# Performance work log

Measured on AMD Instinct MI355X. Metric: run time of the kernel, lower is better.

Reference implementation:

```python
import jax, jax.numpy as jnp
import numpy as np

P = 2        # patch size (all 3 dims)
NB = 8       # num_bands
N = 16       # d_state
DTR = 8      # dt_rank = d_model // 16
DCONV = 4    # d_conv
SMAX = 2.0   # smax_dt = smax_B = smax_C


def _ln(x, g, b):
    mu = x.mean(-1, keepdims=True)
    v = ((x - mu) ** 2).mean(-1, keepdims=True)
    return (x - mu) / jnp.sqrt(v + 1e-5) * g + b


def _silu(x):
    return x * jax.nn.sigmoid(x)


def _ssm_layer(x, band, m, rho, Win, bin_, convw, convb, Wx, Wdt, bdt, Alog, Dp,
               Wout, bout, edt, eB, eC, wr, wm):
    # x: [B, L, d_model] -> bidirectional conditioned selective scan (BiFCSSM)
    Bsz, L, _ = x.shape
    ED = convw.shape[0]
    xz = x @ Win + bin_
    xp, z = xz[..., :ED], xz[..., ED:]
    # depthwise causal conv1d over L
    xpad = jnp.pad(xp, ((0, 0), (DCONV - 1, 0), (0, 0)))
    xc = sum(xpad[:, k:k + L, :] * convw[:, k] for k in range(DCONV)) + convb
    xc = _silu(xc)
    dbl = xc @ Wx                                    # [B,L,DTR+2N]
    dt = jax.nn.softplus(dbl[..., :DTR] @ Wdt + bdt)  # [B,L,ED]
    # band/radius/mask conditioned modulation of delta, B, C
    s_dt = SMAX * jax.nn.sigmoid(edt[band][None] + wr[0] * rho[None] + wm[0] * m)
    s_B = SMAX * jax.nn.sigmoid(eB[band][None] + wr[1] * rho[None] + wm[1] * m)
    s_C = SMAX * jax.nn.sigmoid(eC[band][None] + wr[2] * rho[None] + wm[2] * m)
    dt = dt * s_dt[..., None]
    Bm = dbl[..., DTR:DTR + N] * s_B[..., None]       # [B,L,N]
    Cm = dbl[..., DTR + N:] * s_C[..., None]          # [B,L,N]
    A = -jnp.exp(Alog)                                # [ED,N]
    dA = jnp.exp(dt[..., None] * A)                   # [B,L,ED,N]
    dBu = (dA - 1.0) / A * Bm[:, :, None, :] * xc[..., None]   # exact ZOH
    dA_s = jnp.moveaxis(dA, 1, 0)
    dBu_s = jnp.moveaxis(dBu, 1, 0)
    C_s = jnp.moveaxis(Cm, 1, 0)
    h0 = jnp.zeros((Bsz, ED, N), x.dtype)

    def step(h, inp):
        a, bu, c = inp
        h = a * h + bu
        return h, jnp.einsum('ben,bn->be', h, c)

    _, yf = jax.lax.scan(step, h0, (dA_s, dBu_s, C_s))
    _, yb = jax.lax.scan(step, h0, (dA_s, dBu_s, C_s), reverse=True)
    y = jnp.moveaxis(yf + yb, 0, 1) + Dp * xc
    y = y * _silu(z)
    return y @ Wout + bout


def _fwd(kspace_ri, mask, pe_w, pe_b, pu_w, pu_b, ln_g, ln_b, fn_g, fn_b,
         cond_band, cond_rad_w, cond_mask_w, l0_Win, l0_bin, l0_convw, l0_convb,
         l0_Wx, l0_Wdt, l0_bdt, l0_Alog, l0_D, l0_Wout, l0_bout, l0_edt, l0_eB,
         l0_eC, l0_wr, l0_wm):
    Bsz, C, nx, ny, nz = kspace_ri.shape
    gx, gy, gz = nx // P, ny // P, nz // P
    L = gx * gy * gz
    # patch embed (Conv3d, kernel==stride) as blocked einsum
    xr = kspace_ri.reshape(Bsz, C, gx, P, gy, P, gz, P)
    x = jnp.einsum('bcxiyjzk,dcijk->bdxyz', xr, pe_w) + pe_b[None, :, None, None, None]
    DM = x.shape[1]
    x = x.reshape(Bsz, DM, L).transpose(0, 2, 1)               # [B,L,D]
    m = mask.reshape(Bsz, 1, gx, P, gy, P, gz, P).mean(axis=(3, 5, 7)).reshape(Bsz, L)
    m = jnp.clip(m, 0.0, 1.0)
    # raster scan ordering: identity permutation, rho_bar, band ids
    rho = jnp.arange(L, dtype=x.dtype) / float(L - 1)
    band = jnp.clip(jnp.floor(rho * NB).astype(jnp.int32), 0, NB - 1)
    # condition tokens
    cond = cond_band[band][None] + rho[None, :, None] * cond_rad_w + m[:, :, None] * cond_mask_w
    h = _ln(x + cond, ln_g, ln_b)
    h = h + _ssm_layer(_ln(h, fn_g, fn_b), band, m, rho, l0_Win, l0_bin, l0_convw,
                       l0_convb, l0_Wx, l0_Wdt, l0_bdt, l0_Alog, l0_D, l0_Wout,
                       l0_bout, l0_edt, l0_eB, l0_eC, l0_wr, l0_wm)
    # patch unembed (ConvTranspose3d, kernel==stride) as blocked einsum
    hg = h.transpose(0, 2, 1).reshape(Bsz, DM, gx, gy, gz)
    out = jnp.einsum('bdxyz,dcijk->bcxiyjzk', hg, pu_w).reshape(Bsz, C, nx, ny, nz)
    out = out + pu_b[None, :, None, None, None]
    return kspace_ri + out


def setup_inputs() -> dict:
    key = jax.random.key(0)
    ks = jax.random.split(key, 24)
    ED, DM, CIN = 256, 128, 16

    def nrm(k, shape, s):
        return jax.random.normal(k, shape, jnp.float32) * s

    return {
        'kspace_ri': jax.random.normal(ks[0], (1, CIN, 64, 64, 16), jnp.float32),
        'mask': jax.random.uniform(ks[1], (1, 1, 64, 64, 16), jnp.float32),
        'pe_w': nrm(ks[2], (DM, CIN, P, P, P), 0.09),
        'pe_b': nrm(ks[3], (DM,), 0.02),
        'pu_w': nrm(ks[4], (DM, CIN, P, P, P), 0.05),
        'pu_b': jnp.zeros((CIN,), jnp.float32),
        'ln_g': jnp.ones((DM,), jnp.float32),
        'ln_b': jnp.zeros((DM,), jnp.float32),
        'fn_g': jnp.ones((DM,), jnp.float32),
        'fn_b': jnp.zeros((DM,), jnp.float32),
        'cond_band': nrm(ks[5], (NB, DM), 0.02),
        'cond_rad_w': nrm(ks[6], (DM,), 0.02),
        'cond_mask_w': nrm(ks[7], (DM,), 0.02),
        'l0_Win': nrm(ks[8], (DM, 2 * ED), 0.05),
        'l0_bin': jnp.zeros((2 * ED,), jnp.float32),
        'l0_convw': nrm(ks[9], (ED, DCONV), 0.2),
        'l0_convb': jnp.zeros((ED,), jnp.float32),
        'l0_Wx': nrm(ks[10], (ED, DTR + 2 * N), 0.05),
        'l0_Wdt': nrm(ks[11], (DTR, ED), 0.1),
        'l0_bdt': jnp.full((ED,), -3.0, jnp.float32),
        'l0_Alog': jnp.log(jnp.tile(jnp.arange(1, N + 1, dtype=jnp.float32), (ED, 1))),
        'l0_D': jnp.ones((ED,), jnp.float32),
        'l0_Wout': nrm(ks[12], (ED, DM), 0.05),
        'l0_bout': jnp.zeros((DM,), jnp.float32),
        'l0_edt': nrm(ks[13], (NB,), 0.1),
        'l0_eB': nrm(ks[14], (NB,), 0.1),
        'l0_eC': nrm(ks[15], (NB,), 0.1),
        'l0_wr': nrm(ks[16], (3,), 0.1),
        'l0_wm': nrm(ks[17], (3,), 0.1),
    }


def reference(kspace_ri, mask, pe_w, pe_b, pu_w, pu_b, ln_g, ln_b, fn_g, fn_b,
              cond_band, cond_rad_w, cond_mask_w, l0_Win, l0_bin, l0_convw,
              l0_convb, l0_Wx, l0_Wdt, l0_bdt, l0_Alog, l0_D, l0_Wout, l0_bout,
              l0_edt, l0_eB, l0_eC, l0_wr, l0_wm):
    return _fwd(kspace_ri, mask, pe_w, pe_b, pu_w, pu_b, ln_g, ln_b, fn_g, fn_b,
                cond_band, cond_rad_w, cond_mask_w, l0_Win, l0_bin, l0_convw,
                l0_convb, l0_Wx, l0_Wdt, l0_bdt, l0_Alog, l0_D, l0_Wout, l0_bout,
                l0_edt, l0_eB, l0_eC, l0_wr, l0_wm)
```

## Files before the change

### kernel.cpp

```cpp
#include <hip/hip_runtime.h>
#include <hip/hip_bf16.h>

#define L_TOK 8192
#define NCh 256
#define CLh 32
#define LOG2E 1.44269504088896f

typedef short bf16x8 __attribute__((ext_vector_type(8)));
typedef float f32x4 __attribute__((ext_vector_type(4)));

static __device__ __forceinline__ float nexp2(float x) {
#if __has_builtin(__builtin_amdgcn_exp2f)
    return __builtin_amdgcn_exp2f(x);
#else
    return exp2f(x);
#endif
}
static __device__ __forceinline__ float sigm(float x) {
    return 1.f / (1.f + nexp2(-x * LOG2E));
}

static __device__ __forceinline__ ushort f2bf(float x) {
    union { float f; uint u; } v; v.f = x;
    uint r = v.u + 0x7fffu + ((v.u >> 16) & 1u);
    return (ushort)(r >> 16);
}
static __device__ __forceinline__ float bf2f(ushort h) {
    union { float f; uint u; } v; v.u = ((uint)h) << 16;
    return v.f;
}
static __device__ __forceinline__ void f2hl(float x, ushort* hi, ushort* lo) {
    ushort h = f2bf(x);
    *hi = h;
    *lo = f2bf(x - bf2f(h));
}

// ... 41 lines not shown
        if (n < 256) {
            float s = 0.f;
#pragma unroll
            for (int r = 0; r < 8; ++r) s += Wx[k * 40 + r] * Wdt[r * 256 + n];
            v = s;
        } else if (n < 288) {
            v = Wx[k * 40 + 8 + (n - 256)];
        } else {
            v = 0.f;
        }
    }
    ushort h, lo; f2hl(v, &h, &lo);
    wH[i] = h; wL[i] = lo;
}

__global__ __launch_bounds__(256) void embed_ln_k(const float* __restrict__ ks,
                                                  const ushort* __restrict__ wH, const ushort* __restrict__ wL,
                                                  const float* __restrict__ pe_b, const float* __restrict__ cond_band,
                                                  const float* __restrict__ cond_rad, const float* __restrict__ cond_mask,
                                                  const float* __restrict__ mbuf,
                                                  const float* __restrict__ ln_g, const float* __restrict__ ln_b,
                                                  const float* __restrict__ fn_g, const float* __restrict__ fn_b,
                                                  float* __restrict__ h_,
                                                  ushort* __restrict__ hnH, ushort* __restrict__ hnL) {
    __shared__ __align__(16) char smem[41472];
    ushort (*AsH)[72] = (ushort(*)[72])(smem);
    ushort (*AsL)[72] = (ushort(*)[72])(smem + 2304);
    ushort (*BsH)[72] = (ushort(*)[72])(smem + 4608);
    ushort (*BsL)[72] = (ushort(*)[72])(smem + 23040);
    float  (*Cs)[132] = (float(*)[132])(smem);

    const int tid = threadIdx.x;
    const int lane = tid & 63, wn = tid >> 6;
    const int ln = lane & 15, q = lane >> 4;
    const int mb = blockIdx.x * 16;

    f32x4 acc[2];
    acc[0] = (f32x4){0.f, 0.f, 0.f, 0.f};
    acc[1] = (f32x4){0.f, 0.f, 0.f, 0.f};

    for (int kc = 0; kc < 128; kc += 64) {
        __syncthreads();
        for (int u = tid; u < 1024; u += 256) {
            int r = u >> 6, kk = u & 63;
            int l = mb + r, k = kc + kk;
            int cc = k >> 3, ijk = k & 7;
            int xg = l >> 8, yg = (l >> 3) & 31, zg = l & 7;
            int i2 = (ijk >> 2) & 1, j2 = (ijk >> 1) & 1, k2 = ijk & 1;
// ... 2 lines not shown
            AsH[r][kk] = h; AsL[r][kk] = lo;
        }
        for (int u = tid; u < 1024; u += 256) {
            int n = u >> 3, g = u & 7;
            *(uint4*)&BsH[n][g * 8] = *(const uint4*)&wH[W_PE + n * 128 + kc + g * 8];
            *(uint4*)&BsL[n][g * 8] = *(const uint4*)&wL[W_PE + n * 128 + kc + g * 8];
        }
        __syncthreads();
#pragma unroll
        for (int ks_ = 0; ks_ < 64; ks_ += 32) {
            const int kk = ks_ + q * 8;
            bf16x8 ah = *(const bf16x8*)&AsH[ln][kk];
            bf16x8 al = *(const bf16x8*)&AsL[ln][kk];
#pragma unroll
            for (int cb = 0; cb < 2; ++cb) {
                bf16x8 bh = *(const bf16x8*)&BsH[wn * 32 + cb * 16 + ln][kk];
                bf16x8 bl = *(const bf16x8*)&BsL[wn * 32 + cb * 16 + ln][kk];
                acc[cb] = __builtin_amdgcn_mfma_f32_16x16x32_bf16(ah, bh, acc[cb], 0, 0, 0);
                acc[cb] = __builtin_amdgcn_mfma_f32_16x16x32_bf16(ah, bl, acc[cb], 0, 0, 0);
                acc[cb] = __builtin_amdgcn_mfma_f32_16x16x32_bf16(al, bh, acc[cb], 0, 0, 0);
            }
        }
    }
    __syncthreads();
#pragma unroll
    for (int cb = 0; cb < 2; ++cb) {
#pragma unroll
        for (int r = 0; r < 4; ++r) {
            int row = q * 4 + r;
            int col = wn * 32 + cb * 16 + ln;
            int l = mb + row;
            float rho = (float)l * (1.0f / 8191.0f);
            int band = min(7, (int)(rho * 8.0f));
            Cs[row][col] = acc[cb][r] + pe_b[col] + cond_band[band * 128 + col]
                           + rho * cond_rad[col] + mbuf[l] * cond_mask[col];
        }
    }
    __syncthreads();
    {
        int row = tid >> 4, j = tid & 15;
        int l = mb + row;
        float v8[8];
        float s = 0.f, s2 = 0.f;
#pragma unroll
        for (int i = 0; i < 8; ++i) {
// ... 9 lines not shown
        s = 0.f; s2 = 0.f;
#pragma unroll
        for (int i = 0; i < 8; ++i) {
            int col = j * 8 + i;
            float h = (v8[i] - mu) * rstd * ln_g[col] + ln_b[col];
            hv[i] = h; s += h; s2 += h * h;
        }
#pragma unroll
        for (int i = 0; i < 8; i += 4)
            *(float4*)&h_[(size_t)l * 128 + j * 8 + i] = make_float4(hv[i], hv[i + 1], hv[i + 2], hv[i + 3]);
#pragma unroll
        for (int o = 1; o < 16; o <<= 1) { s += __shfl_xor(s, o, 16); s2 += __shfl_xor(s2, o, 16); }
        mu = s * (1.f / 128.f);
        var = s2 * (1.f / 128.f) - mu * mu;
        rstd = rsqrtf(fmaxf(var, 0.f) + 1e-5f);
        union { ushort u[8]; uint4 v4; } oh, ol;
#pragma unroll
        for (int i = 0; i < 8; ++i) {
            int col = j * 8 + i;
            float o2 = (hv[i] - mu) * rstd * fn_g[col] + fn_b[col];
            ushort hh, ll; f2hl(o2, &hh, &ll);
            oh.u[i] = hh; ol.u[i] = ll;
        }
        *(uint4*)&hnH[(size_t)l * 128 + j * 8] = oh.v4;
        *(uint4*)&hnL[(size_t)l * 128 + j * 8] = ol.v4;
    }
}

__global__ __launch_bounds__(256) void win_k(const ushort* __restrict__ Ah, const ushort* __restrict__ Al,
                                             const ushort* __restrict__ wH, const ushort* __restrict__ wL,
                                             const float* __restrict__ bin_,
                                             float* __restrict__ xp, float* __restrict__ sz) {
    __shared__ ushort AsH[64][72], AsL[64][72];
    __shared__ ushort BsH[64][72], BsL[64][72];
    const int tid = threadIdx.x;
    const int lane = tid & 63, wave = tid >> 6;
    const int wm = wave & 1, wn = wave >> 1;
    const int ln = lane & 15, q = lane >> 4;
    const int mb = blockIdx.x * 64, nb = blockIdx.y * 64;

    f32x4 acc[2][2];
#pragma unroll
    for (int rb = 0; rb < 2; ++rb)
#pragma unroll
        for (int cb = 0; cb < 2; ++cb) acc[rb][cb] = (f32x4){0.f, 0.f, 0.f, 0.f};

    for (int kc = 0; kc < 128; kc += 64) {
        __syncthreads();
        for (int u = tid; u < 512; u += 256) {
            int r = u >> 3, g = u & 7;
            size_t go = (size_t)(mb + r) * 128 + kc + g * 8;
            *(uint4*)&AsH[r][g * 8] = *(const uint4*)&Ah[go];
            *(uint4*)&AsL[r][g * 8] = *(const uint4*)&Al[go];
        }
        for (int u = tid; u < 512; u += 256) {
            int n = u >> 3, g = u & 7;
            size_t go = (size_t)(W_WIN) + (size_t)(nb + n) * 128 + kc + g * 8;
            *(uint4*)&BsH[n][g * 8] = *(const uint4*)&wH[go];
            *(uint4*)&BsL[n][g * 8] = *(const uint4*)&wL[go];
        }
        __syncthreads();
#pragma unroll
        for (int ks_ = 0; ks_ < 64; ks_ += 32) {
            const int kk = ks_ + q * 8;
            bf16x8 ah[2], al[2], bh[2], bl[2];
#pragma unroll
            for (int rb = 0; rb < 2; ++rb) {
                ah[rb] = *(const bf16x8*)&AsH[wm * 32 + rb * 16 + ln][kk];
                al[rb] = *(const bf16x8*)&AsL[wm * 32 + rb * 16 + ln][kk];
            }
#pragma unroll
            for (int cb = 0; cb < 2; ++cb) {
                bh[cb] = *(const bf16x8*)&BsH[wn * 32 + cb * 16 + ln][kk];
                bl[cb] = *(const bf16x8*)&BsL[wn * 32 + cb * 16 + ln][kk];
            }
#pragma unroll
            for (int rb = 0; rb < 2; ++rb)
#pragma unroll
                for (int cb = 0; cb < 2; ++cb) {
                    acc[rb][cb] = __builtin_amdgcn_mfma_f32_16x16x32_bf16(ah[rb], bh[cb], acc[rb][cb], 0, 0, 0);
                    acc[rb][cb] = __builtin_amdgcn_mfma_f32_16x16x32_bf16(ah[rb], bl[cb], acc[rb][cb], 0, 0, 0);
                    acc[rb][cb] = __builtin_amdgcn_mfma_f32_16x16x32_bf16(al[rb], bh[cb], acc[rb][cb], 0, 0, 0);
                }
        }
    }
#pragma unroll
    for (int rb = 0; rb < 2; ++rb)
#pragma unroll
        for (int cb = 0; cb < 2; ++cb)
#pragma unroll
            for (int r = 0; r < 4; ++r) {
                int l = mb + wm * 32 + rb * 16 + q * 4 + r;
                int col = nb + wn * 32 + cb * 16 + ln;
                float v = acc[rb][cb][r] + bin_[col];
                if (col < 256) {
                    xp[(size_t)l * 256 + col] = v;
                } else {
                    sz[(size_t)l * 256 + (col - 256)] = v * sigm(v);
                }
            }
}

__global__ __launch_bounds__(256) void conv_k(const float* __restrict__ xp, const float* __restrict__ convw,
                                              const float* __restrict__ convb, float* __restrict__ xc) {
    int id = blockIdx.x * 256 + threadIdx.x;
    int l = id >> 6, e4 = (id & 63) * 4;
    float4 cw[4];
#pragma unroll
    for (int j = 0; j < 4; ++j) cw[j] = *(const float4*)&convw[(e4 + j) * 4];
    float4 cb = *(const float4*)&convb[e4];
    float o[4] = {cb.x, cb.y, cb.z, cb.w};
#pragma unroll
    for (int k = 0; k < 4; ++k) {
        int lp = l - 3 + k;
        if (lp >= 0) {
// ... 90 lines not shown
                if (col < 256) {
                    float sc0 = 2.0f * sigm(edt[band] + wr[0] * rho + wm[0] * mv);
                    float v2 = v + bdt[col];
                    float sp = (v2 > 20.f) ? v2 : log1pf(expf(v2));
                    dt[(size_t)l * 256 + col] = sp * sc0;
                } else if (col < 272) {
                    float sc1 = 2.0f * sigm(eB[band] + wr[1] * rho + wm[1] * mv);
                    Bm[(size_t)l * 16 + (col - 256)] = v * sc1;
                } else if (col < 288) {
                    float sc2 = 2.0f * sigm(eC[band] + wr[2] * rho + wm[2] * mv);
                    Cm[(size_t)l * 16 + (col - 272)] = v * sc2;
                }
            }
}

template <int PHASE>
__global__ __launch_bounds__(256) void scan_k(const float* __restrict__ dt, const float* __restrict__ xc,
                                              const float* __restrict__ Bm, const float* __restrict__ Cm,
                                              const float* __restrict__ Alog,
                                              float* __restrict__ Hb, float* __restrict__ sdtb,
                                              float* __restrict__ yf, float* __restrict__ yb) {
    const int c = blockIdx.x, dir = blockIdx.y, e = threadIdx.x;
    __shared__ float bms[CLh][16];
    __shared__ float cms[CLh][16];
    for (int idx = e; idx < CLh * 16; idx += 256) {
        bms[idx >> 4][idx & 15] = Bm[c * (CLh * 16) + idx];
        if (PHASE == 1) cms[idx >> 4][idx & 15] = Cm[c * (CLh * 16) + idx];
    }
    float A2[16], iv[16], h[16];
#pragma unroll
    for (int n = 0; n < 16; ++n) {
        float ea = nexp2(Alog[e * 16 + n] * LOG2E);
        A2[n] = -ea * LOG2E;
        iv[n] = -1.0f / ea;
    }
    const size_t hofs = (size_t)(dir * NCh + c) * 4096 + e * 16;
    if (PHASE == 0) {
#pragma unroll
        for (int n = 0; n < 16; ++n) h[n] = 0.f;
    } else {
#pragma unroll
        for (int j = 0; j < 4; ++j) {
            float4 hv = *(const float4*)&Hb[hofs + 4 * j];
            h[4 * j] = hv.x; h[4 * j + 1] = hv.y; h[4 * j + 2] = hv.z; h[4 * j + 3] = hv.w;
        }
    }
    const int base = c * CLh;
    float cu[8], cx[8], nu[8], nx[8];
#pragma unroll
    for (int j = 0; j < 8; ++j) {
        int p = dir ? (CLh - 1 - j) : j;
        cu[j] = dt[(size_t)(base + p) * 256 + e];
        cx[j] = xc[(size_t)(base + p) * 256 + e];
    }
    __syncthreads();
    float sdt = 0.f;
    float* __restrict__ yp = dir ? yb : yf;
#pragma unroll
    for (int g = 0; g < CLh / 8; ++g) {
        if (g + 1 < CLh / 8) {
#pragma unroll
            for (int j = 0; j < 8; ++j) {
                int s = (g + 1) * 8 + j;
                int p = dir ? (CLh - 1 - s) : s;
                nu[j] = dt[(size_t)(base + p) * 256 + e];
                nx[j] = xc[(size_t)(base + p) * 256 + e];
            }
        }
#pragma unroll
        for (int j = 0; j < 8; ++j) {
            int s = g * 8 + j;
            int p = dir ? (CLh - 1 - s) : s;
            float u = cu[j], xv = cx[j];
            union { float4 v[4]; float f[16]; } bb, cc;
            const float4* bp = (const float4*)&bms[p][0];
            bb.v[0] = bp[0]; bb.v[1] = bp[1]; bb.v[2] = bp[2]; bb.v[3] = bp[3];
            if (PHASE == 1) {
                const float4* cp = (const float4*)&cms[p][0];
                cc.v[0] = cp[0]; cc.v[1] = cp[1]; cc.v[2] = cp[2]; cc.v[3] = cp[3];
            }
            float y = 0.f;
#pragma unroll
            for (int n = 0; n < 16; ++n) {
                float a = nexp2(A2[n] * u);
                float w = xv * bb.f[n] * iv[n];
                float t = h[n] + w;
                h[n] = a * t - w;
                if (PHASE == 1) y += h[n] * cc.f[n];
            }
            if (PHASE == 0) sdt += u;
            if (PHASE == 1) yp[(size_t)(base + p) * 256 + e] = y;
        }
#pragma unroll
        for (int j = 0; j < 8; ++j) { cu[j] = nu[j]; cx[j] = nx[j]; }
    }
    if (PHASE == 0) {
#pragma unroll
        for (int j = 0; j < 4; ++j) {
            float4 hv = make_float4(h[4 * j], h[4 * j + 1], h[4 * j + 2], h[4 * j + 3]);
            *(float4*)&Hb[hofs + 4 * j] = hv;
        }
        if (dir == 0) sdtb[c * 256 + e] = sdt;
    }
}

__global__ __launch_bounds__(64) void combine_k(const float* __restrict__ Hb, float* __restrict__ Hpre,
                                                const float* __restrict__ sdtb, const float* __restrict__ Alog) {
    int id = blockIdx.x * 64 + threadIdx.x;
    int dir = id >> 12, en = id & 4095, e = en >> 4;
    float A2 = -nexp2(Alog[en] * LOG2E) * LOG2E;
    float hi = 0.f;
    for (int g = 0; g < NCh / 8; ++g) {
        float Pv[8], qv[8];
#pragma unroll
        for (int j = 0; j < 8; ++j) {
            int c = dir ? (NCh - 1 - (g * 8 + j)) : (g * 8 + j);
            Pv[j] = sdtb[c * 256 + e];
            qv[j] = Hb[(size_t)(dir * NCh + c) * 4096 + en];
        }
#pragma unroll
        for (int j = 0; j < 8; ++j) {
            int c = dir ? (NCh - 1 - (g * 8 + j)) : (g * 8 + j);
            float P = nexp2(A2 * Pv[j]);
            Hpre[(size_t)(dir * NCh + c) * 4096 + en] = hi;
            hi = P * hi + qv[j];
        }
    }
}

__global__ __launch_bounds__(256) void wout_k(const float* __restrict__ yf, const float* __restrict__ yb,
                                              const float* __restrict__ xc, const float* __restrict__ sz,
                                              const float* __restrict__ Dp,
                                              const ushort* __restrict__ wH, const ushort* __restrict__ wL,
                                              const float* __restrict__ bout, const float* __restrict__ h_,
                                              ushort* __restrict__ hfH, ushort* __restrict__ hfL) {
    __shared__ ushort AsH[32][72], AsL[32][72];
    __shared__ ushort BsH[64][72], BsL[64][72];
    const int tid = threadIdx.x;
    const int lane = tid & 63, wave = tid >> 6;
    const int wm = wave & 1, wn = wave >> 1;
    const int ln = lane & 15, q = lane >> 4;
    const int mb = blockIdx.x * 32, nb = blockIdx.y * 64;

    f32x4 acc[2];
    acc[0] = (f32x4){0.f, 0.f, 0.f, 0.f};
    acc[1] = (f32x4){0.f, 0.f, 0.f, 0.f};

    for (int kc = 0; kc < 256; kc += 64) {
        __syncthreads();
        for (int u = tid; u < 512; u += 256) {
            int r = u >> 4, kq = u & 15;
            size_t go = (size_t)(mb + r) * 256 + kc + kq * 4;
            float4 a = *(const float4*)&yf[go];
            float4 b = *(const float4*)&yb[go];
            float4 x = *(const float4*)&xc[go];
            float4 s = *(const float4*)&sz[go];
            float4 d = *(const float4*)&Dp[kc + kq * 4];
            float v0 = (a.x + b.x + d.x * x.x) * s.x;
            float v1 = (a.y + b.y + d.y * x.y) * s.y;
            float v2 = (a.z + b.z + d.z * x.z) * s.z;
            float v3 = (a.w + b.w + d.w * x.w) * s.w;
            union { ushort u[4]; uint2 v2; } hh, ll;
            f2hl(v0, &hh.u[0], &ll.u[0]); f2hl(v1, &hh.u[1], &ll.u[1]);
            f2hl(v2, &hh.u[2], &ll.u[2]); f2hl(v3, &hh.u[3], &ll.u[3]);
            *(uint2*)&AsH[r][kq * 4] = hh.v2;
            *(uint2*)&AsL[r][kq * 4] = ll.v2;
        }
        for (int u = tid; u < 512; u += 256) {
            int n = u >> 3, g = u & 7;
            size_t go = (size_t)(W_WOUT) + (size_t)(nb + n) * 256 + kc + g * 8;
            *(uint4*)&BsH[n][g * 8] = *(const uint4*)&wH[go];
            *(uint4*)&BsL[n][g * 8] = *(const uint4*)&wL[go];
        }
        __syncthreads();
#pragma unroll
        for (int ks_ = 0; ks_ < 64; ks_ += 32) {
            const int kk = ks_ + q * 8;
            bf16x8 ah = *(const bf16x8*)&AsH[wm * 16 + ln][kk];
            bf16x8 al = *(const bf16x8*)&AsL[wm * 16 + ln][kk];
#pragma unroll
            for (int cb = 0; cb < 2; ++cb) {
                bf16x8 bh = *(const bf16x8*)&BsH[wn * 32 + cb * 16 + ln][kk];
                bf16x8 bl = *(const bf16x8*)&BsL[wn * 32 + cb * 16 + ln][kk];
                acc[cb] = __builtin_amdgcn_mfma_f32_16x16x32_bf16(ah, bh, acc[cb], 0, 0, 0);
                acc[cb] = __builtin_amdgcn_mfma_f32_16x16x32_bf16(ah, bl, acc[cb], 0, 0, 0);
                acc[cb] = __builtin_amdgcn_mfma_f32_16x16x32_bf16(al, bh, acc[cb], 0, 0, 0);
            }
        }
    }
#pragma unroll
    for (int cb = 0; cb < 2; ++cb)
#pragma unroll
        for (int r = 0; r < 4; ++r) {
            int l = mb + wm * 16 + q * 4 + r;
            int col = nb + wn * 32 + cb * 16 + ln;
            float v = acc[cb][r] + bout[col] + h_[(size_t)l * 128 + col];
            ushort hh, ll; f2hl(v, &hh, &ll);
            hfH[(size_t)l * 128 + col] = hh;
            hfL[(size_t)l * 128 + col] = ll;
        }
}

__global__ __launch_bounds__(256) void unembed_k(const ushort* __restrict__ Ah, const ushort* __restrict__ Al,
                                                 const ushort* __restrict__ wH, const ushort* __restrict__ wL,
                                                 const float* __restrict__ pu_b, const float* __restrict__ ks,
                                                 float* __restrict__ out) {
    __shared__ ushort AsH[32][72], AsL[32][72];
    __shared__ ushort BsH[64][72], BsL[64][72];
    const int tid = threadIdx.x;
    const int lane = tid & 63, wave = tid >> 6;
    const int wm = wave & 1, wn = wave >> 1;
    const int ln = lane & 15, q = lane >> 4;
    const int mb = blockIdx.x * 32, nb = blockIdx.y * 64;

    f32x4 acc[2];
    acc[0] = (f32x4){0.f, 0.f, 0.f, 0.f};
    acc[1] = (f32x4){0.f, 0.f, 0.f, 0.f};

    for (int kc = 0; kc < 128; kc += 64) {
        __syncthreads();
        for (int u = tid; u < 256; u += 256) {
            int r = u >> 3, g = u & 7;
            size_t go = (size_t)(mb + r) * 128 + kc + g * 8;
            *(uint4*)&AsH[r][g * 8] = *(const uint4*)&Ah[go];
            *(uint4*)&AsL[r][g * 8] = *(const uint4*)&Al[go];
        }
        for (int u = tid; u < 512; u += 256) {
            int n = u >> 3, g = u & 7;
            size_t go = (size_t)(W_PU) + (size_t)(nb + n) * 128 + kc + g * 8;
            *(uint4*)&BsH[n][g * 8] = *(const uint4*)&wH[go];
            *(uint4*)&BsL[n][g * 8] = *(const uint4*)&wL[go];
        }
        __syncthreads();
#pragma unroll
        for (int ks_ = 0; ks_ < 64; ks_ += 32) {
            const int kk = ks_ + q * 8;
            bf16x8 ah = *(const bf16x8*)&AsH[wm * 16 + ln][kk];
            bf16x8 al = *(const bf16x8*)&AsL[wm * 16 + ln][kk];
#pragma unroll
            for (int cb = 0; cb < 2; ++cb) {
                bf16x8 bh = *(const bf16x8*)&BsH[wn * 32 + cb * 16 + ln][kk];
                bf16x8 bl = *(const bf16x8*)&BsL[wn * 32 + cb * 16 + ln][kk];
                acc[cb] = __builtin_amdgcn_mfma_f32_16x16x32_bf16(ah, bh, acc[cb], 0, 0, 0);
                acc[cb] = __builtin_amdgcn_mfma_f32_16x16x32_bf16(ah, bl, acc[cb], 0, 0, 0);
                acc[cb] = __builtin_amdgcn_mfma_f32_16x16x32_bf16(al, bh, acc[cb], 0, 0, 0);
            }
        }
    }
#pragma unroll
    for (int cb = 0; cb < 2; ++cb)
#pragma unroll
        for (int r = 0; r < 4; ++r) {
            int l = mb + wm * 16 + q * 4 + r;
            int col = nb + wn * 32 + cb * 16 + ln;
            int xg = l >> 8, yg = (l >> 3) & 31, zg = l & 7;
            int c = col >> 3, ijk = col & 7;
            int i2 = (ijk >> 2) & 1, j2 = (ijk >> 1) & 1, k2 = ijk & 1;
            size_t idx = (size_t)((c * 64 + 2 * xg + i2) * 64 + (2 * yg + j2)) * 16 + 2 * zg + k2;
            out[idx] = acc[cb][r] + pu_b[c] + ks[idx];
        }
}

extern "C" void kernel_launch(void* const* d_in, const int* in_sizes, int n_in,
                              void* d_out, int out_size, void* d_ws, size_t ws_size,
                              hipStream_t stream) {
    const float* ks    = (const float*)d_in[0];
    const float* mask  = (const float*)d_in[1];
    const float* pe_w  = (const float*)d_in[2];
    const float* pe_b  = (const float*)d_in[3];
    const float* pu_w  = (const float*)d_in[4];
    const float* pu_b  = (const float*)d_in[5];
    const float* ln_g  = (const float*)d_in[6];
    const float* ln_b  = (const float*)d_in[7];
    const float* fn_g  = (const float*)d_in[8];
    const float* fn_b  = (const float*)d_in[9];
// ... 13 lines not shown
    const float* bout  = (const float*)d_in[23];
    const float* edt   = (const float*)d_in[24];
    const float* eB    = (const float*)d_in[25];
    const float* eC    = (const float*)d_in[26];
    const float* wr    = (const float*)d_in[27];
    const float* wm    = (const float*)d_in[28];
    float* out = (float*)d_out;

    char* base = (char*)d_ws;
    size_t o = 0;
    auto alloc = [&](size_t bytes) { char* p = base + o; o += (bytes + 255) & ~(size_t)255; return p; };
    float*  mbuf = (float*)alloc(32768);
    ushort* wH   = (ushort*)alloc(W_TOT * 2);
    ushort* wL   = (ushort*)alloc(W_TOT * 2);
    float*  h_   = (float*)alloc(4194304);
    ushort* hnH  = (ushort*)alloc(2097152);
    ushort* hnL  = (ushort*)alloc(2097152);
    float*  xp   = (float*)alloc(8388608);
    float*  sz   = (float*)alloc(8388608);
    float*  xc   = (float*)alloc(8388608);
    float*  dt   = (float*)alloc(8388608);
    float*  Bm   = (float*)alloc(524288);
    float*  Cm   = (float*)alloc(524288);
    float*  Hb   = (float*)alloc(8388608);
    float*  Hpre = (float*)alloc(8388608);
    float*  sdtb = (float*)alloc(262144);
    float*  yf   = (float*)alloc(8388608);
    float*  yb   = (float*)alloc(8388608);
    ushort* hfH  = (ushort*)alloc(2097152);
    ushort* hfL  = (ushort*)alloc(2097152);

    prep_k<<<864, 256, 0, stream>>>(pe_w, Win, Wx, Wdt, Wout, pu_w, mask, wH, wL, mbuf);
    embed_ln_k<<<512, 256, 0, stream>>>(ks, wH, wL, pe_b, cond_band, cond_rad, cond_mask, mbuf,
                                        ln_g, ln_b, fn_g, fn_b, h_, hnH, hnL);
    win_k<<<dim3(128, 8), 256, 0, stream>>>(hnH, hnL, wH, wL, bin_, xp, sz);
    conv_k<<<2048, 256, 0, stream>>>(xp, convw, convb, xc);
    proj_k<<<dim3(128, 5), 256, 0, stream>>>(xc, wH, wL, bdt, mbuf, edt, eB, eC, wr, wm, dt, Bm, Cm);
    scan_k<0><<<dim3(NCh, 2), 256, 0, stream>>>(dt, xc, Bm, Cm, Alog, Hb, sdtb, nullptr, nullptr);
    combine_k<<<128, 64, 0, stream>>>(Hb, Hpre, sdtb, Alog);
    scan_k<1><<<dim3(NCh, 2), 256, 0, stream>>>(dt, xc, Bm, Cm, Alog, Hpre, sdtb, yf, yb);
    wout_k<<<dim3(256, 2), 256, 0, stream>>>(yf, yb, xc, sz, Dp, wH, wL, bout, h_, hfH, hfL);
    unembed_k<<<dim3(256, 2), 256, 0, stream>>>(hfH, hfL, wH, wL, pu_b, ks, out);
}
```

Baseline: 239.9 us.

## Fuse embed+Win GEMM and scan phase 1 with Wout and unembed GEMMs

Merges the embedding/LayerNorm kernel with the Win projection so normalized activations stay in shared memory instead of round-tripping through global hi/lo buffers. It also fuses the second scan phase with the output projection and unembedding in one 512-thread block per chunk, where both scan directions run concurrently and are summed in LDS. This removes the yf/yb/hn/hf intermediate buffers and three launches. In exchange, tail_k runs only 256 blocks with heavy register use, and it reads Wout/pu weights straight from global memory rather than staging them in shared memory.

```diff
diff --git a/kernel.cpp b/kernel.cpp
--- a/kernel.cpp
+++ b/kernel.cpp
@@ -19,7 +19,6 @@
 static __device__ __forceinline__ float sigm(float x) {
     return 1.f / (1.f + nexp2(-x * LOG2E));
 }
-
 static __device__ __forceinline__ ushort f2bf(float x) {
     union { float f; uint u; } v; v.f = x;
     uint r = v.u + 0x7fffu + ((v.u >> 16) & 1u);
@@ -91,24 +90,29 @@
     wH[i] = h; wL[i] = lo;
 }
 
-__global__ __launch_bounds__(256) void embed_ln_k(const float* __restrict__ ks,
-                                                  const ushort* __restrict__ wH, const ushort* __restrict__ wL,
-                                                  const float* __restrict__ pe_b, const float* __restrict__ cond_band,
-                                                  const float* __restrict__ cond_rad, const float* __restrict__ cond_mask,
-                                                  const float* __restrict__ mbuf,
-                                                  const float* __restrict__ ln_g, const float* __restrict__ ln_b,
-                                                  const float* __restrict__ fn_g, const float* __restrict__ fn_b,
-                                                  float* __restrict__ h_,
-                                                  ushort* __restrict__ hnH, ushort* __restrict__ hnL) {
-    __shared__ __align__(16) char smem[41472];
+__global__ __launch_bounds__(256) void front_k(const float* __restrict__ ks,
+                                               const ushort* __restrict__ wH, const ushort* __restrict__ wL,
+                                               const float* __restrict__ pe_b, const float* __restrict__ cond_band,
+                                               const float* __restrict__ cond_rad, const float* __restrict__ cond_mask,
+                                               const float* __restrict__ mbuf,
+                                               const float* __restrict__ ln_g, const float* __restrict__ ln_b,
+                                               const float* __restrict__ fn_g, const float* __restrict__ fn_b,
+                                               const float* __restrict__ bin_,
+                                               float* __restrict__ h_,
+                                               float* __restrict__ xp, float* __restrict__ sz) {
+    __shared__ __align__(16) char smem[51968];
     ushort (*AsH)[72] = (ushort(*)[72])(smem);
     ushort (*AsL)[72] = (ushort(*)[72])(smem + 2304);
     ushort (*BsH)[72] = (ushort(*)[72])(smem + 4608);
     ushort (*BsL)[72] = (ushort(*)[72])(smem + 23040);
-    float  (*Cs)[132] = (float(*)[132])(smem);
+    float  (*Cs)[132]  = (float(*)[132])(smem);
+    ushort (*hnH)[136] = (ushort(*)[136])(smem + 8448);
+    ushort (*hnL)[136] = (ushort(*)[136])(smem + 12800);
+    ushort (*BwH)[136] = (ushort(*)[136])(smem + 17152);
+    ushort (*BwL)[136] = (ushort(*)[136])(smem + 34560);
 
     const int tid = threadIdx.x;
-    const int lane = tid & 63, wn = tid >> 6;
+    const int lane = tid & 63, wv = tid >> 6;
     const int ln = lane & 15, q = lane >> 4;
     const int mb = blockIdx.x * 16;
 
@@ -141,8 +145,8 @@
             bf16x8 al = *(const bf16x8*)&AsL[ln][kk];
 #pragma unroll
             for (int cb = 0; cb < 2; ++cb) {
-                bf16x8 bh = *(const bf16x8*)&BsH[wn * 32 + cb * 16 + ln][kk];
-                bf16x8 bl = *(const bf16x8*)&BsL[wn * 32 + cb * 16 + ln][kk];
+                bf16x8 bh = *(const bf16x8*)&BsH[wv * 32 + cb * 16 + ln][kk];
+                bf16x8 bl = *(const bf16x8*)&BsL[wv * 32 + cb * 16 + ln][kk];
                 acc[cb] = __builtin_amdgcn_mfma_f32_16x16x32_bf16(ah, bh, acc[cb], 0, 0, 0);
                 acc[cb] = __builtin_amdgcn_mfma_f32_16x16x32_bf16(ah, bl, acc[cb], 0, 0, 0);
                 acc[cb] = __builtin_amdgcn_mfma_f32_16x16x32_bf16(al, bh, acc[cb], 0, 0, 0);
@@ -155,7 +159,7 @@
 #pragma unroll
         for (int r = 0; r < 4; ++r) {
             int row = q * 4 + r;
-            int col = wn * 32 + cb * 16 + ln;
+            int col = wv * 32 + cb * 16 + ln;
             int l = mb + row;
             float rho = (float)l * (1.0f / 8191.0f);
             int band = min(7, (int)(rho * 8.0f));
@@ -195,91 +199,47 @@
         mu = s * (1.f / 128.f);
         var = s2 * (1.f / 128.f) - mu * mu;
         rstd = rsqrtf(fmaxf(var, 0.f) + 1e-5f);
-        union { ushort u[8]; uint4 v4; } oh, ol;
 #pragma unroll
         for (int i = 0; i < 8; ++i) {
             int col = j * 8 + i;
             float o2 = (hv[i] - mu) * rstd * fn_g[col] + fn_b[col];
             ushort hh, ll; f2hl(o2, &hh, &ll);
-            oh.u[i] = hh; ol.u[i] = ll;
-        }
-        *(uint4*)&hnH[(size_t)l * 128 + j * 8] = oh.v4;
-        *(uint4*)&hnL[(size_t)l * 128 + j * 8] = ol.v4;
-    }
-}
-
-__global__ __launch_bounds__(256) void win_k(const ushort* __restrict__ Ah, const ushort* __restrict__ Al,
-                                             const ushort* __restrict__ wH, const ushort* __restrict__ wL,
-                                             const float* __restrict__ bin_,
-                                             float* __restrict__ xp, float* __restrict__ sz) {
-    __shared__ ushort AsH[64][72], AsL[64][72];
-    __shared__ ushort BsH[64][72], BsL[64][72];
-    const int tid = threadIdx.x;
-    const int lane = tid & 63, wave = tid >> 6;
-    const int wm = wave & 1, wn = wave >> 1;
-    const int ln = lane & 15, q = lane >> 4;
-    const int mb = blockIdx.x * 64, nb = blockIdx.y * 64;
-
-    f32x4 acc[2][2];
-#pragma unroll
-    for (int rb = 0; rb < 2; ++rb)
-#pragma unroll
-        for (int cb = 0; cb < 2; ++cb) acc[rb][cb] = (f32x4){0.f, 0.f, 0.f, 0.f};
-
-    for (int kc = 0; kc < 128; kc += 64) {
-        __syncthreads();
-        for (int u = tid; u < 512; u += 256) {
-            int r = u >> 3, g = u & 7;
-            size_t go = (size_t)(mb + r) * 128 + kc + g * 8;
-            *(uint4*)&AsH[r][g * 8] = *(const uint4*)&Ah[go];
-            *(uint4*)&AsL[r][g * 8] = *(const uint4*)&Al[go];
-        }
-        for (int u = tid; u < 512; u += 256) {
-            int n = u >> 3, g = u & 7;
-            size_t go = (size_t)(W_WIN) + (size_t)(nb + n) * 128 + kc + g * 8;
-            *(uint4*)&BsH[n][g * 8] = *(const uint4*)&wH[go];
-            *(uint4*)&BsL[n][g * 8] = *(const uint4*)&wL[go];
-        }
-        __syncthreads();
-#pragma unroll
-        for (int ks_ = 0; ks_ < 64; ks_ += 32) {
-            const int kk = ks_ + q * 8;
-            bf16x8 ah[2], al[2], bh[2], bl[2];
-#pragma unroll
-            for (int rb = 0; rb < 2; ++rb) {
-                ah[rb] = *(const bf16x8*)&AsH[wm * 32 + rb * 16 + ln][kk];
-                al[rb] = *(const bf16x8*)&AsL[wm * 32 + rb * 16 + ln][kk];
-            }
-#pragma unroll
-            for (int cb = 0; cb < 2; ++cb) {
-                bh[cb] = *(const bf16x8*)&BsH[wn * 32 + cb * 16 + ln][kk];
-                bl[cb] = *(const bf16x8*)&BsL[wn * 32 + cb * 16 + ln][kk];
-            }
-#pragma unroll
-            for (int rb = 0; rb < 2; ++rb)
-#pragma unroll
-                for (int cb = 0; cb < 2; ++cb) {
-                    acc[rb][cb] = __builtin_amdgcn_mfma_f32_16x16x32_bf16(ah[rb], bh[cb], acc[rb][cb], 0, 0, 0);
-                    acc[rb][cb] = __builtin_amdgcn_mfma_f32_16x16x32_bf16(ah[rb], bl[cb], acc[rb][cb], 0, 0, 0);
-                    acc[rb][cb] = __builtin_amdgcn_mfma_f32_16x16x32_bf16(al[rb], bh[cb], acc[rb][cb], 0, 0, 0);
-                }
-        }
-    }
-#pragma unroll
-    for (int rb = 0; rb < 2; ++rb)
-#pragma unroll
-        for (int cb = 0; cb < 2; ++cb)
-#pragma unroll
-            for (int r = 0; r < 4; ++r) {
-                int l = mb + wm * 32 + rb * 16 + q * 4 + r;
-                int col = nb + wn * 32 + cb * 16 + ln;
-                float v = acc[rb][cb][r] + bin_[col];
-                if (col < 256) {
-                    xp[(size_t)l * 256 + col] = v;
-                } else {
-                    sz[(size_t)l * 256 + (col - 256)] = v * sigm(v);
-                }
-            }
+            hnH[row][col] = hh; hnL[row][col] = ll;
+        }
+    }
+    for (int nt = 0; nt < 8; ++nt) {
+        __syncthreads();
+        for (int u = tid; u < 1024; u += 256) {
+            int n = u >> 4, g = u & 15;
+            size_t go = (size_t)(W_WIN) + (size_t)(nt * 64 + n) * 128 + g * 8;
+            *(uint4*)&BwH[n][g * 8] = *(const uint4*)&wH[go];
+            *(uint4*)&BwL[n][g * 8] = *(const uint4*)&wL[go];
+        }
+        __syncthreads();
+        f32x4 wa = (f32x4){0.f, 0.f, 0.f, 0.f};
+#pragma unroll
+        for (int kst = 0; kst < 4; ++kst) {
+            const int kk = kst * 32 + q * 8;
+            bf16x8 ah = *(const bf16x8*)&hnH[ln][kk];
+            bf16x8 al = *(const bf16x8*)&hnL[ln][kk];
+            bf16x8 bh = *(const bf16x8*)&BwH[wv * 16 + ln][kk];
+            bf16x8 bl = *(const bf16x8*)&BwL[wv * 16 + ln][kk];
+            wa = __builtin_amdgcn_mfma_f32_16x16x32_bf16(ah, bh, wa, 0, 0, 0);
+            wa = __builtin_amdgcn_mfma_f32_16x16x32_bf16(ah, bl, wa, 0, 0, 0);
+            wa = __builtin_amdgcn_mfma_f32_16x16x32_bf16(al, bh, wa, 0, 0, 0);
+        }
+#pragma unroll
+        for (int r = 0; r < 4; ++r) {
+            int l = mb + q * 4 + r;
+            int col = nt * 64 + wv * 16 + ln;
+            float v = wa[r] + bin_[col];
+            if (col < 256) {
+                xp[(size_t)l * 256 + col] = v;
+            } else {
+                sz[(size_t)l * 256 + (col - 256)] = v * sigm(v);
+            }
+        }
+    }
 }
 
 __global__ __launch_bounds__(256) void conv_k(const float* __restrict__ xp, const float* __restrict__ convw,
@@ -400,36 +360,20 @@
             }
 }
 
-template <int PHASE>
-__global__ __launch_bounds__(256) void scan_k(const float* __restrict__ dt, const float* __restrict__ xc,
-                                              const float* __restrict__ Bm, const float* __restrict__ Cm,
-                                              const float* __restrict__ Alog,
-                                              float* __restrict__ Hb, float* __restrict__ sdtb,
-                                              float* __restrict__ yf, float* __restrict__ yb) {
+__global__ __launch_bounds__(256) void scan0_k(const float* __restrict__ dt, const float* __restrict__ xc,
+                                               const float* __restrict__ Bm, const float* __restrict__ Alog,
+                                               float* __restrict__ Hb, float* __restrict__ sdtb) {
     const int c = blockIdx.x, dir = blockIdx.y, e = threadIdx.x;
     __shared__ float bms[CLh][16];
-    __shared__ float cms[CLh][16];
-    for (int idx = e; idx < CLh * 16; idx += 256) {
+    for (int idx = e; idx < CLh * 16; idx += 256)
         bms[idx >> 4][idx & 15] = Bm[c * (CLh * 16) + idx];
-        if (PHASE == 1) cms[idx >> 4][idx & 15] = Cm[c * (CLh * 16) + idx];
-    }
     float A2[16], iv[16], h[16];
 #pragma unroll
     for (int n = 0; n < 16; ++n) {
         float ea = nexp2(Alog[e * 16 + n] * LOG2E);
         A2[n] = -ea * LOG2E;
         iv[n] = -1.0f / ea;
-    }
-    const size_t hofs = (size_t)(dir * NCh + c) * 4096 + e * 16;
-    if (PHASE == 0) {
-#pragma unroll
-        for (int n = 0; n < 16; ++n) h[n] = 0.f;
-    } else {
-#pragma unroll
-        for (int j = 0; j < 4; ++j) {
-            float4 hv = *(const float4*)&Hb[hofs + 4 * j];
-            h[4 * j] = hv.x; h[4 * j + 1] = hv.y; h[4 * j + 2] = hv.z; h[4 * j + 3] = hv.w;
-        }
+        h[n] = 0.f;
     }
     const int base = c * CLh;
     float cu[8], cx[8], nu[8], nx[8];
@@ -441,7 +385,6 @@
     }
     __syncthreads();
     float sdt = 0.f;
-    float* __restrict__ yp = dir ? yb : yf;
 #pragma unroll
     for (int g = 0; g < CLh / 8; ++g) {
         if (g + 1 < CLh / 8) {
@@ -458,36 +401,25 @@
             int s = g * 8 + j;
             int p = dir ? (CLh - 1 - s) : s;
             float u = cu[j], xv = cx[j];
-            union { float4 v[4]; float f[16]; } bb, cc;
+            union { float4 v[4]; float f[16]; } bb;
             const float4* bp = (const float4*)&bms[p][0];
             bb.v[0] = bp[0]; bb.v[1] = bp[1]; bb.v[2] = bp[2]; bb.v[3] = bp[3];
-            if (PHASE == 1) {
-                const float4* cp = (const float4*)&cms[p][0];
-                cc.v[0] = cp[0]; cc.v[1] = cp[1]; cc.v[2] = cp[2]; cc.v[3] = cp[3];
-            }
-            float y = 0.f;
 #pragma unroll
             for (int n = 0; n < 16; ++n) {
                 float a = nexp2(A2[n] * u);
                 float w = xv * bb.f[n] * iv[n];
-                float t = h[n] + w;
-                h[n] = a * t - w;
-                if (PHASE == 1) y += h[n] * cc.f[n];
-            }
-            if (PHASE == 0) sdt += u;
-            if (PHASE == 1) yp[(size_t)(base + p) * 256 + e] = y;
+                h[n] = a * (h[n] + w) - w;
+            }
+            sdt += u;
         }
 #pragma unroll
         for (int j = 0; j < 8; ++j) { cu[j] = nu[j]; cx[j] = nx[j]; }
     }
-    if (PHASE == 0) {
-#pragma unroll
-        for (int j = 0; j < 4; ++j) {
-            float4 hv = make_float4(h[4 * j], h[4 * j + 1], h[4 * j + 2], h[4 * j + 3]);
-            *(float4*)&Hb[hofs + 4 * j] = hv;
-        }
-        if (dir == 0) sdtb[c * 256 + e] = sdt;
-    }
+    const size_t hofs = (size_t)(dir * NCh + c) * 4096 + e * 16;
+#pragma unroll
+    for (int j = 0; j < 4; ++j)
+        *(float4*)&Hb[hofs + 4 * j] = make_float4(h[4 * j], h[4 * j + 1], h[4 * j + 2], h[4 * j + 3]);
+    if (dir == 0) sdtb[c * 256 + e] = sdt;
 }
 
 __global__ __launch_bounds__(64) void combine_k(const float* __restrict__ Hb, float* __restrict__ Hpre,
@@ -514,137 +446,157 @@
     }
 }
 
-__global__ __launch_bounds__(256) void wout_k(const float* __restrict__ yf, const float* __restrict__ yb,
-                                              const float* __restrict__ xc, const float* __restrict__ sz,
-                                              const float* __restrict__ Dp,
+__global__ __launch_bounds__(512) void tail_k(const float* __restrict__ dt, const float* __restrict__ xc,
+                                              const float* __restrict__ Bm, const float* __restrict__ Cm,
+                                              const float* __restrict__ Alog, const float* __restrict__ Hpre,
+                                              const float* __restrict__ sz, const float* __restrict__ Dp,
                                               const ushort* __restrict__ wH, const ushort* __restrict__ wL,
                                               const float* __restrict__ bout, const float* __restrict__ h_,
-                                              ushort* __restrict__ hfH, ushort* __restrict__ hfL) {
-    __shared__ ushort AsH[32][72], AsL[32][72];
-    __shared__ ushort BsH[64][72], BsL[64][72];
+                                              const float* __restrict__ pu_b, const float* __restrict__ ks,
+                                              float* __restrict__ out) {
+    __shared__ float bms[CLh][16];
+    __shared__ float cms[CLh][16];
+    __shared__ __align__(16) char sm2[33792];
+    float  (*ysum)[256] = (float(*)[256])(sm2);
+    ushort (*AH)[272]   = (ushort(*)[272])(sm2 + 16384);
+    ushort (*AL)[272]   = (ushort(*)[272])(sm2 + 25088);
+    ushort (*hfH)[136]  = (ushort(*)[136])(sm2);
+    ushort (*hfL)[136]  = (ushort(*)[136])(sm2 + 4352);
+
+    const int c = blockIdx.x;
     const int tid = threadIdx.x;
-    const int lane = tid & 63, wave = tid >> 6;
-    const int wm = wave & 1, wn = wave >> 1;
+    const int dir = tid >> 8;
+    const int e = tid & 255;
+    const int wave = tid >> 6, lane = tid & 63;
     const int ln = lane & 15, q = lane >> 4;
-    const int mb = blockIdx.x * 32, nb = blockIdx.y * 64;
-
-    f32x4 acc[2];
-    acc[0] = (f32x4){0.f, 0.f, 0.f, 0.f};
-    acc[1] = (f32x4){0.f, 0.f, 0.f, 0.f};
-
-    for (int kc = 0; kc < 256; kc += 64) {
-        __syncthreads();
-        for (int u = tid; u < 512; u += 256) {
-            int r = u >> 4, kq = u & 15;
-            size_t go = (size_t)(mb + r) * 256 + kc + kq * 4;
-            float4 a = *(const float4*)&yf[go];
-            float4 b = *(const float4*)&yb[go];
-            float4 x = *(const float4*)&xc[go];
-            float4 s = *(const float4*)&sz[go];
-            float4 d = *(const float4*)&Dp[kc + kq * 4];
-            float v0 = (a.x + b.x + d.x * x.x) * s.x;
-            float v1 = (a.y + b.y + d.y * x.y) * s.y;
-            float v2 = (a.z + b.z + d.z * x.z) * s.z;
-            float v3 = (a.w + b.w + d.w * x.w) * s.w;
-            union { ushort u[4]; uint2 v2; } hh, ll;
-            f2hl(v0, &hh.u[0], &ll.u[0]); f2hl(v1, &hh.u[1], &ll.u[1]);
-            f2hl(v2, &hh.u[2], &ll.u[2]); f2hl(v3, &hh.u[3], &ll.u[3]);
-            *(uint2*)&AsH[r][kq * 4] = hh.v2;
-            *(uint2*)&AsL[r][kq * 4] = ll.v2;
-        }
-        for (int u = tid; u < 512; u += 256) {
-            int n = u >> 3, g = u & 7;
-            size_t go = (size_t)(W_WOUT) + (size_t)(nb + n) * 256 + kc + g * 8;
-            *(uint4*)&BsH[n][g * 8] = *(const uint4*)&wH[go];
-            *(uint4*)&BsL[n][g * 8] = *(const uint4*)&wL[go];
-        }
-        __syncthreads();
-#pragma unroll
-        for (int ks_ = 0; ks_ < 64; ks_ += 32) {
-            const int kk = ks_ + q * 8;
-            bf16x8 ah = *(const bf16x8*)&AsH[wm * 16 + ln][kk];
-            bf16x8 al = *(const bf16x8*)&AsL[wm * 16 + ln][kk];
-#pragma unroll
-            for (int cb = 0; cb < 2; ++cb) {
-                bf16x8 bh = *(const bf16x8*)&BsH[wn * 32 + cb * 16 + ln][kk];
-                bf16x8 bl = *(const bf16x8*)&BsL[wn * 32 + cb * 16 + ln][kk];
-                acc[cb] = __builtin_amdgcn_mfma_f32_16x16x32_bf16(ah, bh, acc[cb], 0, 0, 0);
-                acc[cb] = __builtin_amdgcn_mfma_f32_16x16x32_bf16(ah, bl, acc[cb], 0, 0, 0);
-                acc[cb] = __builtin_amdgcn_mfma_f32_16x16x32_bf16(al, bh, acc[cb], 0, 0, 0);
-            }
-        }
-    }
-#pragma unroll
-    for (int cb = 0; cb < 2; ++cb)
+
+    for (int idx = tid; idx < CLh * 16; idx += 512) {
+        bms[idx >> 4][idx & 15] = Bm[c * (CLh * 16) + idx];
+        cms[idx >> 4][idx & 15] = Cm[c * (CLh * 16) + idx];
+    }
+    float A2[16], iv[16], h[16];
+#pragma unroll
+    for (int n = 0; n < 16; ++n) {
+        float ea = nexp2(Alog[e * 16 + n] * LOG2E);
+        A2[n] = -ea * LOG2E;
+        iv[n] = -1.0f / ea;
+    }
+    const size_t hofs = (size_t)(dir * NCh + c) * 4096 + e * 16;
+#pragma unroll
+    for (int j = 0; j < 4; ++j) {
+        float4 hv = *(const float4*)&Hpre[hofs + 4 * j];
+        h[4 * j] = hv.x; h[4 * j + 1] = hv.y; h[4 * j + 2] = hv.z; h[4 * j + 3] = hv.w;
+    }
+    const int base = c * CLh;
+    float yreg[CLh];
+    float cu[8], cx[8], nu[8], nx[8];
+#pragma unroll
+    for (int j = 0; j < 8; ++j) {
+        int p = dir ? (CLh - 1 - j) : j;
+        cu[j] = dt[(size_t)(base + p) * 256 + e];
+        cx[j] = xc[(size_t)(base + p) * 256 + e];
+    }
+    __syncthreads();
+#pragma unroll
+    for (int g = 0; g < CLh / 8; ++g) {
+        if (g + 1 < CLh / 8) {
+#pragma unroll
+            for (int j = 0; j < 8; ++j) {
+                int s = (g + 1) * 8 + j;
+                int p = dir ? (CLh - 1 - s) : s;
+                nu[j] = dt[(size_t)(base + p) * 256 + e];
+                nx[j] = xc[(size_t)(base + p) * 256 + e];
+            }
+        }
+#pragma unroll
+        for (int j = 0; j < 8; ++j) {
+            int s = g * 8 + j;
+            int p = dir ? (CLh - 1 - s) : s;
+            float u = cu[j], xv = cx[j];
+            union { float4 v[4]; float f[16]; } bb, cc;
+            const float4* bp = (const float4*)&bms[p][0];
+            bb.v[0] = bp[0]; bb.v[1] = bp[1]; bb.v[2] = bp[2]; bb.v[3] = bp[3];
+            const float4* cp = (const float4*)&cms[p][0];
+            cc.v[0] = cp[0]; cc.v[1] = cp[1]; cc.v[2] = cp[2]; cc.v[3] = cp[3];
+            float y = 0.f;
+#pragma unroll
+            for (int n = 0; n < 16; ++n) {
+                float a = nexp2(A2[n] * u);
+                float w = xv * bb.f[n] * iv[n];
+                h[n] = a * (h[n] + w) - w;
+                y += h[n] * cc.f[n];
+            }
+            yreg[p] = y;
+        }
+#pragma unroll
+        for (int j = 0; j < 8; ++j) { cu[j] = nu[j]; cx[j] = nx[j]; }
+    }
+
+    float dpv = Dp[e];
+#pragma unroll
+    for (int half = 0; half < 2; ++half) {
+        __syncthreads();
+        if (dir == 0) {
+#pragma unroll
+            for (int l = 0; l < 16; ++l) ysum[l][e] = yreg[half * 16 + l];
+        }
+        __syncthreads();
+        if (dir == 1) {
+#pragma unroll
+            for (int l = 0; l < 16; ++l) {
+                size_t gl = (size_t)(base + half * 16 + l) * 256 + e;
+                float a = (ysum[l][e] + yreg[half * 16 + l] + dpv * xc[gl]) * sz[gl];
+                ushort hh, ll; f2hl(a, &hh, &ll);
+                AH[l][e] = hh; AL[l][e] = ll;
+            }
+        }
+        __syncthreads();
+        f32x4 wa = (f32x4){0.f, 0.f, 0.f, 0.f};
+#pragma unroll
+        for (int kst = 0; kst < 8; ++kst) {
+            const int kk = kst * 32 + q * 8;
+            bf16x8 ah = *(const bf16x8*)&AH[ln][kk];
+            bf16x8 al = *(const bf16x8*)&AL[ln][kk];
+            bf16x8 bh = *(const bf16x8*)&wH[W_WOUT + (size_t)(wave * 16 + ln) * 256 + kk];
+            bf16x8 bl = *(const bf16x8*)&wL[W_WOUT + (size_t)(wave * 16 + ln) * 256 + kk];
+            wa = __builtin_amdgcn_mfma_f32_16x16x32_bf16(ah, bh, wa, 0, 0, 0);
+            wa = __builtin_amdgcn_mfma_f32_16x16x32_bf16(ah, bl, wa, 0, 0, 0);
+            wa = __builtin_amdgcn_mfma_f32_16x16x32_bf16(al, bh, wa, 0, 0, 0);
+        }
+        __syncthreads();
 #pragma unroll
         for (int r = 0; r < 4; ++r) {
-            int l = mb + wm * 16 + q * 4 + r;
-            int col = nb + wn * 32 + cb * 16 + ln;
-            float v = acc[cb][r] + bout[col] + h_[(size_t)l * 128 + col];
+            int l16 = q * 4 + r;
+            int col = wave * 16 + ln;
+            int l = base + half * 16 + l16;
+            float v = wa[r] + bout[col] + h_[(size_t)l * 128 + col];
             ushort hh, ll; f2hl(v, &hh, &ll);
-            hfH[(size_t)l * 128 + col] = hh;
-            hfL[(size_t)l * 128 + col] = ll;
-        }
-}
-
-__global__ __launch_bounds__(256) void unembed_k(const ushort* __restrict__ Ah, const ushort* __restrict__ Al,
-                                                 const ushort* __restrict__ wH, const ushort* __restrict__ wL,
-                                                 const float* __restrict__ pu_b, const float* __restrict__ ks,
-                                                 float* __restrict__ out) {
-    __shared__ ushort AsH[32][72], AsL[32][72];
-    __shared__ ushort BsH[64][72], BsL[64][72];
-    const int tid = threadIdx.x;
-    const int lane = tid & 63, wave = tid >> 6;
-    const int wm = wave & 1, wn = wave >> 1;
-    const int ln = lane & 15, q = lane >> 4;
-    const int mb = blockIdx.x * 32, nb = blockIdx.y * 64;
-
-    f32x4 acc[2];
-    acc[0] = (f32x4){0.f, 0.f, 0.f, 0.f};
-    acc[1] = (f32x4){0.f, 0.f, 0.f, 0.f};
-
-    for (int kc = 0; kc < 128; kc += 64) {
-        __syncthreads();
-        for (int u = tid; u < 256; u += 256) {
-            int r = u >> 3, g = u & 7;
-            size_t go = (size_t)(mb + r) * 128 + kc + g * 8;
-            *(uint4*)&AsH[r][g * 8] = *(const uint4*)&Ah[go];
-            *(uint4*)&AsL[r][g * 8] = *(const uint4*)&Al[go];
-        }
-        for (int u = tid; u < 512; u += 256) {
-            int n = u >> 3, g = u & 7;
-            size_t go = (size_t)(W_PU) + (size_t)(nb + n) * 128 + kc + g * 8;
-            *(uint4*)&BsH[n][g * 8] = *(const uint4*)&wH[go];
-            *(uint4*)&BsL[n][g * 8] = *(const uint4*)&wL[go];
-        }
-        __syncthreads();
-#pragma unroll
-        for (int ks_ = 0; ks_ < 64; ks_ += 32) {
-            const int kk = ks_ + q * 8;
-            bf16x8 ah = *(const bf16x8*)&AsH[wm * 16 + ln][kk];
-            bf16x8 al = *(const bf16x8*)&AsL[wm * 16 + ln][kk];
-#pragma unroll
-            for (int cb = 0; cb < 2; ++cb) {
-                bf16x8 bh = *(const bf16x8*)&BsH[wn * 32 + cb * 16 + ln][kk];
-                bf16x8 bl = *(const bf16x8*)&BsL[wn * 32 + cb * 16 + ln][kk];
-                acc[cb] = __builtin_amdgcn_mfma_f32_16x16x32_bf16(ah, bh, acc[cb], 0, 0, 0);
-                acc[cb] = __builtin_amdgcn_mfma_f32_16x16x32_bf16(ah, bl, acc[cb], 0, 0, 0);
-                acc[cb] = __builtin_amdgcn_mfma_f32_16x16x32_bf16(al, bh, acc[cb], 0, 0, 0);
-            }
-        }
-    }
-#pragma unroll
-    for (int cb = 0; cb < 2; ++cb)
+            hfH[l16][col] = hh; hfL[l16][col] = ll;
+        }
+        __syncthreads();
+        f32x4 ua = (f32x4){0.f, 0.f, 0.f, 0.f};
+#pragma unroll
+        for (int kst = 0; kst < 4; ++kst) {
+            const int kk = kst * 32 + q * 8;
+            bf16x8 ah = *(const bf16x8*)&hfH[ln][kk];
+            bf16x8 al = *(const bf16x8*)&hfL[ln][kk];
+            bf16x8 bh = *(const bf16x8*)&wH[W_PU + (size_t)(wave * 16 + ln) * 128 + kk];
+            bf16x8 bl = *(const bf16x8*)&wL[W_PU + (size_t)(wave * 16 + ln) * 128 + kk];
+            ua = __builtin_amdgcn_mfma_f32_16x16x32_bf16(ah, bh, ua, 0, 0, 0);
+            ua = __builtin_amdgcn_mfma_f32_16x16x32_bf16(ah, bl, ua, 0, 0, 0);
+            ua = __builtin_amdgcn_mfma_f32_16x16x32_bf16(al, bh, ua, 0, 0, 0);
+        }
 #pragma unroll
         for (int r = 0; r < 4; ++r) {
-            int l = mb + wm * 16 + q * 4 + r;
-            int col = nb + wn * 32 + cb * 16 + ln;
+            int l = base + half * 16 + q * 4 + r;
+            int col = wave * 16 + ln;
             int xg = l >> 8, yg = (l >> 3) & 31, zg = l & 7;
-            int c = col >> 3, ijk = col & 7;
+            int cc = col >> 3, ijk = col & 7;
             int i2 = (ijk >> 2) & 1, j2 = (ijk >> 1) & 1, k2 = ijk & 1;
-            size_t idx = (size_t)((c * 64 + 2 * xg + i2) * 64 + (2 * yg + j2)) * 16 + 2 * zg + k2;
-            out[idx] = acc[cb][r] + pu_b[c] + ks[idx];
-        }
+            size_t idx = (size_t)((cc * 64 + 2 * xg + i2) * 64 + (2 * yg + j2)) * 16 + 2 * zg + k2;
+            out[idx] = ua[r] + pu_b[cc] + ks[idx];
+        }
+    }
 }
 
 extern "C" void kernel_launch(void* const* d_in, const int* in_sizes, int n_in,
@@ -688,8 +640,6 @@
     ushort* wH   = (ushort*)alloc(W_TOT * 2);
     ushort* wL   = (ushort*)alloc(W_TOT * 2);
     float*  h_   = (float*)alloc(4194304);
-    ushort* hnH  = (ushort*)alloc(2097152);
-    ushort* hnL  = (ushort*)alloc(2097152);
     float*  xp   = (float*)alloc(8388608);
     float*  sz   = (float*)alloc(8388608);
     float*  xc   = (float*)alloc(8388608);
@@ -699,20 +649,13 @@
     float*  Hb   = (float*)alloc(8388608);
     float*  Hpre = (float*)alloc(8388608);
     float*  sdtb = (float*)alloc(262144);
-    float*  yf   = (float*)alloc(8388608);
-    float*  yb   = (float*)alloc(8388608);
-    ushort* hfH  = (ushort*)alloc(2097152);
-    ushort* hfL  = (ushort*)alloc(2097152);
 
     prep_k<<<864, 256, 0, stream>>>(pe_w, Win, Wx, Wdt, Wout, pu_w, mask, wH, wL, mbuf);
-    embed_ln_k<<<512, 256, 0, stream>>>(ks, wH, wL, pe_b, cond_band, cond_rad, cond_mask, mbuf,
-                                        ln_g, ln_b, fn_g, fn_b, h_, hnH, hnL);
-    win_k<<<dim3(128, 8), 256, 0, stream>>>(hnH, hnL, wH, wL, bin_, xp, sz);
+    front_k<<<512, 256, 0, stream>>>(ks, wH, wL, pe_b, cond_band, cond_rad, cond_mask, mbuf,
+                                     ln_g, ln_b, fn_g, fn_b, bin_, h_, xp, sz);
     conv_k<<<2048, 256, 0, stream>>>(xp, convw, convb, xc);
     proj_k<<<dim3(128, 5), 256, 0, stream>>>(xc, wH, wL, bdt, mbuf, edt, eB, eC, wr, wm, dt, Bm, Cm);
-    scan_k<0><<<dim3(NCh, 2), 256, 0, stream>>>(dt, xc, Bm, Cm, Alog, Hb, sdtb, nullptr, nullptr);
+    scan0_k<<<dim3(NCh, 2), 256, 0, stream>>>(dt, xc, Bm, Alog, Hb, sdtb);
     combine_k<<<128, 64, 0, stream>>>(Hb, Hpre, sdtb, Alog);
-    scan_k<1><<<dim3(NCh, 2), 256, 0, stream>>>(dt, xc, Bm, Cm, Alog, Hpre, sdtb, yf, yb);
-    wout_k<<<dim3(256, 2), 256, 0, stream>>>(yf, yb, xc, sz, Dp, wH, wL, bout, h_, hfH, hfL);
-    unembed_k<<<dim3(256, 2), 256, 0, stream>>>(hfH, hfL, wH, wL, pu_b, ks, out);
-}
+    tail_k<<<NCh, 512, 0, stream>>>(dt, xc, Bm, Cm, Alog, Hpre, sz, Dp, wH, wL, bout, h_, pu_b, ks, out);
+}
```

After: 338.5 us. 41.1% more time.
